# Kernel tuning notes

Measured on AMD Instinct MI355X. Metric: run time of the kernel, lower is better.

Reference implementation:

```python
import jax, jax.numpy as jnp
import numpy as np

N, E, G = 200000, 800000, 8192
IN, H, D, EXTRA = 128, 4, 64, 16


def setup_inputs() -> dict:
    key = jax.random.key(0)
    ks = jax.random.split(key, 24)
    inp = {
        'feats_node': jax.random.normal(ks[0], (N, IN), jnp.float32),
        'feats_graph': jax.random.normal(ks[1], (G, EXTRA), jnp.float32),
        'src': jax.random.randint(ks[2], (E,), 0, N, jnp.int32),
        'dst': jax.random.randint(ks[3], (E,), 0, N, jnp.int32),
        'graph_ids': jnp.sort(jax.random.randint(ks[4], (N,), 0, G, jnp.int32)),
        # GAT layer 1: fc [H*D, IN], attn [H, D], bias zeros (DGL default)
        'fc1_w': 0.5 * jax.random.normal(ks[5], (H * D, IN), jnp.float32),
        'attn_l1': 0.5 * jax.random.normal(ks[6], (H, D), jnp.float32),
        'attn_r1': 0.5 * jax.random.normal(ks[7], (H, D), jnp.float32),
        'bias1': jnp.zeros((H * D,), jnp.float32),
        # GAT layer 2
        'fc2_w': 0.5 * jax.random.normal(ks[8], (H * D, H * D), jnp.float32),
        'attn_l2': 0.5 * jax.random.normal(ks[9], (H, D), jnp.float32),
        'attn_r2': 0.5 * jax.random.normal(ks[10], (H, D), jnp.float32),
        'bias2': jnp.zeros((H * D,), jnp.float32),
        # GAT layer 3: 1 head
        'fc3_w': 0.5 * jax.random.normal(ks[11], (D, H * D), jnp.float32),
        'attn_l3': 0.5 * jax.random.normal(ks[12], (1, D), jnp.float32),
        'attn_r3': 0.5 * jax.random.normal(ks[13], (1, D), jnp.float32),
        'bias3': jnp.zeros((D,), jnp.float32),
        # readout score
        'score_w': 0.5 * jax.random.normal(ks[14], (1, D), jnp.float32),
        'score_b': jnp.zeros((1,), jnp.float32),
        # MLP: [D+EXTRA -> 2D -> D -> 1]
        'mlp_w1': 0.5 * jax.random.normal(ks[15], (2 * D, D + EXTRA), jnp.float32),
        'mlp_b1': jnp.zeros((2 * D,), jnp.float32),
        'mlp_w2': 0.5 * jax.random.normal(ks[16], (D, 2 * D), jnp.float32),
        'mlp_b2': jnp.zeros((D,), jnp.float32),
        'mlp_w3': 0.5 * jax.random.normal(ks[17], (1, D), jnp.float32),
        'mlp_b3': jnp.zeros((1,), jnp.float32),
    }
    return inp


def gat_conv(x, src, dst, fc_w, attn_l, attn_r, bias, n_heads, out_dim):
    # DGL GATConv: proj -> edge leaky_relu attention -> per-dst softmax -> aggregate
    n = x.shape[0]
    feat = (x @ fc_w.T).reshape(n, n_heads, out_dim)          # [N,H,D]
    el = jnp.einsum('nhd,hd->nh', feat, attn_l)               # [N,H]
    er = jnp.einsum('nhd,hd->nh', feat, attn_r)
    e = jax.nn.leaky_relu(el[src] + er[dst], 0.2)             # [E,H]
    m = jax.ops.segment_max(e, dst, num_segments=n)           # per-dst max
    m = jax.lax.stop_gradient(jnp.where(jnp.isfinite(m), m, 0.0))
    a = jnp.exp(e - m[dst])                                   # [E,H]
    denom = jax.ops.segment_sum(a, dst, num_segments=n)       # [N,H]
    alpha = a / jnp.where(denom[dst] == 0, 1.0, denom[dst])
    out = jax.ops.segment_sum(alpha[:, :, None] * feat[src], dst, num_segments=n)
    return out + bias.reshape(1, n_heads, out_dim)            # [N,H,D]


def reference(feats_node, feats_graph, src, dst, graph_ids,
              fc1_w, attn_l1, attn_r1, bias1,
              fc2_w, attn_l2, attn_r2, bias2,
              fc3_w, attn_l3, attn_r3, bias3,
              score_w, score_b,
              mlp_w1, mlp_b1, mlp_w2, mlp_b2, mlp_w3, mlp_b3):
    n = feats_node.shape[0]
    g = feats_graph.shape[0]
    x = jax.nn.selu(gat_conv(feats_node, src, dst, fc1_w, attn_l1, attn_r1, bias1, H, D)).reshape(n, H * D)
    x = jax.nn.selu(gat_conv(x, src, dst, fc2_w, attn_l2, attn_r2, bias2, H, D)).reshape(n, H * D)
    x = jax.nn.selu(gat_conv(x, src, dst, fc3_w, attn_l3, attn_r3, bias3, 1, D)).reshape(n, D)
    # weighted-average readout: sum(w*x)/sum(w) per graph
    w = jax.nn.sigmoid(x @ score_w.T + score_b)               # [N,1]
    num = jax.ops.segment_sum(w * x, graph_ids, num_segments=g)
    den = jax.ops.segment_sum(w, graph_ids, num_segments=g)
    emb = num / jnp.where(den == 0, 1.0, den)                 # [G,D]
    z = jnp.concatenate([emb, feats_graph], axis=1)           # [G,D+EXTRA]
    h = jax.nn.selu(z @ mlp_w1.T + mlp_b1)
    h = jax.nn.selu(h @ mlp_w2.T + mlp_b2)
    return h @ mlp_w3.T + mlp_b3                              # [G,1]
```

## Files before the change

kernel.cpp:

```cpp
#include <hip/hip_runtime.h>
#include <math.h>

#define N_NODES 200000
#define N_EDGES 800000
#define N_GRAPHS 8192
#define B1 16
#define B2 8
#define EC 128

typedef unsigned short ushort_t;

__device__ __forceinline__ float selu_f(float x){
  const float alpha = 1.6732632423543772f;
  const float lam   = 1.0507009873554805f;
  return x > 0.f ? lam * x : lam * alpha * (expf(x) - 1.f);
}

__global__ void zero_i32(int* p, int n){
  int i = blockIdx.x * 256 + threadIdx.x;
  if (i < n) p[i] = 0;
}

__global__ void deg_kernel(const int* __restrict__ dst, int* __restrict__ deg, int E){
  int e = blockIdx.x * 256 + threadIdx.x;
  if (e < E) atomicAdd(&deg[dst[e]], 1);
}

__global__ void scan1(const int* __restrict__ deg, int* __restrict__ rp, int* __restrict__ bs, int n){
  __shared__ int sh[256];
  int t = threadIdx.x;
  int base = blockIdx.x * 1024;
  int v[4]; int s = 0;
  #pragma unroll
  for (int i = 0; i < 4; i++){
    int idx = base + t * 4 + i;
    v[i] = (idx < n) ? deg[idx] : 0;
    s += v[i];
  }
  sh[t] = s; __syncthreads();
  for (int off = 1; off < 256; off <<= 1){
    int x = (t >= off) ? sh[t - off] : 0;
    __syncthreads();
    sh[t] += x;
    __syncthreads();
  }
  int run = (t == 0) ? 0 : sh[t - 1];
  #pragma unroll
  for (int i = 0; i < 4; i++){
    int idx = base + t * 4 + i;
    if (idx < n) rp[idx] = run;
    run += v[i];
  }
  if (t == 255) bs[blockIdx.x] = sh[255];
}

__global__ void scan2(int* bs, int nb){
  __shared__ int sh[256];
  int t = threadIdx.x;
  sh[t] = (t < nb) ? bs[t] : 0; __syncthreads();
  for (int off = 1; off < 256; off <<= 1){
    int x = (t >= off) ? sh[t - off] : 0;
    __syncthreads();
    sh[t] += x;
    __syncthreads();
  }
  int excl = (t == 0) ? 0 : sh[t - 1];
  if (t < nb) bs[t] = excl;
}

__global__ void scan3(int* rp, const int* __restrict__ bs, int n, int total){
  int i = blockIdx.x * 256 + threadIdx.x;
  if (i < n) rp[i] += bs[i >> 10];
  if (i == 0) rp[n] = total;
}

__global__ void fill_csr(const int* __restrict__ src, const int* __restrict__ dst,
                         const int* __restrict__ rp, int* __restrict__ fil,
                         int* __restrict__ csr, int E){
  int e = blockIdx.x * 256 + threadIdx.x;
  if (e < E){
    int d = dst[e];
    int p = atomicAdd(&fil[d], 1);
    csr[rp[d] + p] = src[e];
  }
}

__global__ void wt_kernel(const float* __restrict__ W1, const float* __restrict__ W2,
                          const float* __restrict__ W3,
                          float* __restrict__ W1t, float* __restrict__ W2t,
                          float* __restrict__ W3t){
  int i = blockIdx.x * 256 + threadIdx.x;
  if (i < 32768){
    int k = i >> 8, m = i & 255;
    W1t[i] = W1[(size_t)m * 128 + k];
  } else if (i < 32768 + 65536){
    int j = i - 32768;
    int k = j >> 8, m = j & 255;
    W2t[j] = W2[(size_t)m * 256 + k];
  } else if (i < 32768 + 65536 + 16384){
    int j = i - 32768 - 65536;
    int k = j >> 6, c = j & 63;
    W3t[j] = W3[(size_t)c * 256 + k];
  }
}

__global__ void compute_v(const float* __restrict__ W1, const float* __restrict__ al1, const float* __restrict__ ar1,
                          const float* __restrict__ W2, const float* __restrict__ al2, const float* __restrict__ ar2,
                          const float* __restrict__ W3, const float* __restrict__ al3, const float* __restrict__ ar3,
                          float* __restrict__ V1L, float* __restrict__ V1R,
                          float* __restrict__ V2L, float* __restrict__ V2R,
                          float* __restrict__ V3L, float* __restrict__ V3R){
  int i = blockIdx.x * 256 + threadIdx.x;
  if (i < 512){
    int h = i >> 7, k = i & 127;
    float sl = 0.f, sr = 0.f;
    for (int dd = 0; dd < 64; dd++){
      float w = W1[(size_t)(h * 64 + dd) * 128 + k];
      sl += al1[h * 64 + dd] * w;
      sr += ar1[h * 64 + dd] * w;
    }
    V1L[i] = sl; V1R[i] = sr;
  } else if (i < 1536){
    int j = i - 512;
    int h = j >> 8, k = j & 255;
    float sl = 0.f, sr = 0.f;
    for (int dd = 0; dd < 64; dd++){
      float w = W2[(size_t)(h * 64 + dd) * 256 + k];
      sl += al2[h * 64 + dd] * w;
      sr += ar2[h * 64 + dd] * w;
    }
    V2L[j] = sl; V2R[j] = sr;
  } else if (i < 1792){
    int k = i - 1536;
    float sl = 0.f, sr = 0.f;
    for (int dd = 0; dd < 64; dd++){
      float w = W3[(size_t)dd * 256 + k];
      sl += al3[dd] * w;
      sr += ar3[dd] * w;
    }
    V3L[k] = sl; V3R[k] = sr;
  }
}

__global__ __launch_bounds__(256) void el_er1(const float* __restrict__ x0,
                                              const float* __restrict__ V1L, const float* __restrict__ V1R,
                                              float* __restrict__ el1, float* __restrict__ er1, int n){
  __shared__ float vl[512], vr[512];
  int t = threadIdx.x;
  for (int i = t; i < 512; i += 256){ vl[i] = V1L[i]; vr[i] = V1R[i]; }
  __syncthreads();
  int node = blockIdx.x * 4 + (t >> 6);
  int l = t & 63;
  if (node >= n) return;
  float xa = x0[(size_t)node * 128 + l];
  float xb = x0[(size_t)node * 128 + 64 + l];
  #pragma unroll
  for (int h = 0; h < 4; h++){
    float pl = xa * vl[h * 128 + l] + xb * vl[h * 128 + 64 + l];
    float pr = xa * vr[h * 128 + l] + xb * vr[h * 128 + 64 + l];
    #pragma unroll
    for (int off = 32; off; off >>= 1){ pl += __shfl_xor(pl, off); pr += __shfl_xor(pr, off); }
    if (l == 0){ el1[(size_t)node * 4 + h] = pl; er1[(size_t)node * 4 + h] = pr; }
  }
}

__global__ __launch_bounds__(256) void alpha_h4(const float* __restrict__ el, const float* __restrict__ er,
                                                const int* __restrict__ rp, const int* __restrict__ csr,
                                                float* __restrict__ a, int n){
  int node = blockIdx.x * 256 + threadIdx.x;
  if (node >= n) return;
  int s0 = rp[node], s1 = rp[node + 1];
  if (s0 >= s1) return;
  float4 erv = *reinterpret_cast<const float4*>(er + (size_t)node * 4);
  float m0 = -1e30f, m1 = -1e30f, m2 = -1e30f, m3 = -1e30f;
  for (int i = s0; i < s1; i++){
    float4 e = *reinterpret_cast<const float4*>(el + (size_t)csr[i] * 4);
    float e0 = e.x + erv.x; e0 = e0 > 0.f ? e0 : 0.2f * e0; m0 = fmaxf(m0, e0);
    float e1 = e.y + erv.y; e1 = e1 > 0.f ? e1 : 0.2f * e1; m1 = fmaxf(m1, e1);
    float e2 = e.z + erv.z; e2 = e2 > 0.f ? e2 : 0.2f * e2; m2 = fmaxf(m2, e2);
    float e3 = e.w + erv.w; e3 = e3 > 0.f ? e3 : 0.2f * e3; m3 = fmaxf(m3, e3);
  }
  float d0 = 0.f, d1 = 0.f, d2 = 0.f, d3 = 0.f;
  for (int i = s0; i < s1; i++){
    float4 e = *reinterpret_cast<const float4*>(el + (size_t)csr[i] * 4);
    float e0 = e.x + erv.x; e0 = e0 > 0.f ? e0 : 0.2f * e0; d0 += expf(e0 - m0);
    float e1 = e.y + erv.y; e1 = e1 > 0.f ? e1 : 0.2f * e1; d1 += expf(e1 - m1);
    float e2 = e.z + erv.z; e2 = e2 > 0.f ? e2 : 0.2f * e2; d2 += expf(e2 - m2);
    float e3 = e.w + erv.w; e3 = e3 > 0.f ? e3 : 0.2f * e3; d3 += expf(e3 - m3);
  }
  d0 = 1.f / d0; d1 = 1.f / d1; d2 = 1.f / d2; d3 = 1.f / d3;
  for (int i = s0; i < s1; i++){
    float4 e = *reinterpret_cast<const float4*>(el + (size_t)csr[i] * 4);
    float4 o;
    float e0 = e.x + erv.x; e0 = e0 > 0.f ? e0 : 0.2f * e0; o.x = expf(e0 - m0) * d0;
    float e1 = e.y + erv.y; e1 = e1 > 0.f ? e1 : 0.2f * e1; o.y = expf(e1 - m1) * d1;
    float e2 = e.z + erv.z; e2 = e2 > 0.f ? e2 : 0.2f * e2; o.z = expf(e2 - m2) * d2;
    float e3 = e.w + erv.w; e3 = e3 > 0.f ? e3 : 0.2f * e3; o.w = expf(e3 - m3) * d3;
    *reinterpret_cast<float4*>(a + (size_t)i * 4) = o;
  }
}

__global__ __launch_bounds__(256) void alpha_h1(const float* __restrict__ el, const float* __restrict__ er,
                                                const int* __restrict__ rp, const int* __restrict__ csr,
                                                float* __restrict__ a, int n){
  int node = blockIdx.x * 256 + threadIdx.x;
  if (node >= n) return;
  int s0 = rp[node], s1 = rp[node + 1];
  if (s0 >= s1) return;
  float erv = er[node];
  float m = -1e30f;
  for (int i = s0; i < s1; i++){
    float e = el[csr[i]] + erv; e = e > 0.f ? e : 0.2f * e; m = fmaxf(m, e);
  }
  float den = 0.f;
  for (int i = s0; i < s1; i++){
    float e = el[csr[i]] + erv; e = e > 0.f ? e : 0.2f * e; den += expf(e - m);
  }
  float inv = 1.f / den;
  for (int i = s0; i < s1; i++){
    float e = el[csr[i]] + erv; e = e > 0.f ? e : 0.2f * e; a[i] = expf(e - m) * inv;
  }
}

__global__ __launch_bounds__(512, 2) void l1_fused(
    const float* __restrict__ x0, const float* __restrict__ W1t, const float* __restrict__ bias1,
    const float* __restrict__ a1,
    const float* __restrict__ V2L, const float* __restrict__ V2R,
    const int* __restrict__ rp, const int* __restrict__ csr,
    ushort_t* __restrict__ x1hi, unsigned char* __restrict__ x1lo,
    float* __restrict__ el2, float* __restrict__ er2){
  __shared__ float  aggT[4][129][20];
  __shared__ float  x1s[16][260];
  __shared__ float4 als4[EC];
  __shared__ int    ssrc[EC];
  __shared__ int    rpc[B1 + 1];
  int t = threadIdx.x;
  int nb0 = blockIdx.x * B1;
  if (t <= B1) rpc[t] = rp[nb0 + t];
  __syncthreads();
  int e0 = rpc[0], eN = rpc[B1];

  {
    int c = t & 127, g = t >> 7;
    float accr[4][4] = {{0.f}};
    for (int c0 = e0; c0 < eN; c0 += EC){
      int ce = min(EC, eN - c0);
      for (int i = t; i < ce; i += 512){
        ssrc[i] = csr[c0 + i];
        als4[i] = *reinterpret_cast<const float4*>(a1 + (size_t)(c0 + i) * 4);
      }
      __syncthreads();
      #pragma unroll
      for (int dd = 0; dd < 4; dd++){
        int d = g + dd * 4;
        int lo = max(rpc[d], c0) - c0;
        int hi = min(rpc[d + 1], c0 + ce) - c0;
        for (int i = lo; i < hi; i++){
          float xv = x0[(size_t)ssrc[i] * 128 + c];
          float4 av = als4[i];
          accr[dd][0] += av.x * xv;
          accr[dd][1] += av.y * xv;
          accr[dd][2] += av.z * xv;
          accr[dd][3] += av.w * xv;
        }
      }
      __syncthreads();
    }
    #pragma unroll
    for (int dd = 0; dd < 4; dd++){
      int d = g + dd * 4;
      aggT[0][c][d] = accr[dd][0];
      aggT[1][c][d] = accr[dd][1];
      aggT[2][c][d] = accr[dd][2];
      aggT[3][c][d] = accr[dd][3];
    }
  }
  __syncthreads();

  if (t < 256){
    int mt = t & 63, dt = t >> 6;
    int m0 = mt * 4, d0 = dt * 4, h = mt >> 4;
    float acc[4][4] = {{0.f}};
    #pragma unroll 4
    for (int k = 0; k < 128; k++){
      float4 w = *reinterpret_cast<const float4*>(W1t + (size_t)k * 256 + m0);
      float4 a = *reinterpret_cast<const float4*>(&aggT[h][k][d0]);
      acc[0][0] += a.x * w.x; acc[0][1] += a.x * w.y; acc[0][2] += a.x * w.z; acc[0][3] += a.x * w.w;
      acc[1][0] += a.y * w.x; acc[1][1] += a.y * w.y; acc[1][2] += a.y * w.z; acc[1][3] += a.y * w.w;
      acc[2][0] += a.z * w.x; acc[2][1] += a.z * w.y; acc[2][2] += a.z * w.z; acc[2][3] += a.z * w.w;
      acc[3][0] += a.w * w.x; acc[3][1] += a.w * w.y; acc[3][2] += a.w * w.z; acc[3][3] += a.w * w.w;
    }
    float4 b = *reinterpret_cast<const float4*>(bias1 + m0);
    #pragma unroll
    for (int i = 0; i < 4; i++){
      float4 v;
      v.x = selu_f(acc[i][0] + b.x);
      v.y = selu_f(acc[i][1] + b.y);
      v.z = selu_f(acc[i][2] + b.z);
      v.w = selu_f(acc[i][3] + b.w);
      *reinterpret_cast<float4*>(&x1s[d0 + i][m0]) = v;
      unsigned int ux = __float_as_uint(v.x), uy = __float_as_uint(v.y);
      unsigned int uz = __float_as_uint(v.z), uw = __float_as_uint(v.w);
      ushort4 h4; uchar4 l4;
      h4.x = (ushort_t)(ux >> 16); h4.y = (ushort_t)(uy >> 16);
      h4.z = (ushort_t)(uz >> 16); h4.w = (ushort_t)(uw >> 16);
      l4.x = (unsigned char)(ux >> 8); l4.y = (unsigned char)(uy >> 8);
      l4.z = (unsigned char)(uz >> 8); l4.w = (unsigned char)(uw >> 8);
      size_t base = (size_t)(nb0 + d0 + i) * 256 + m0;
      *reinterpret_cast<ushort4*>(x1hi + base) = h4;
      *reinterpret_cast<uchar4*>(x1lo + base) = l4;
    }
  }
  __syncthreads();

  if (t < 128){
    int d = t & 15, hq = (t >> 4) & 3, lr = t >> 6;
    const float* V = lr ? V2R : V2L;
    float p = 0.f;
    for (int k = 0; k < 256; k++) p += V[hq * 256 + k] * x1s[d][k];
    if (lr) er2[(size_t)(nb0 + d) * 4 + hq] = p;
    else    el2[(size_t)(nb0 + d) * 4 + hq] = p;
  }
}

__global__ __launch_bounds__(512, 2) void l2_fused(
    const ushort_t* __restrict__ x1hi, const unsigned char* __restrict__ x1lo,
    const float* __restrict__ W2t, const float* __restrict__ bias2,
    const float* __restrict__ a2, const float* __restrict__ W3t,
    const float* __restrict__ V3L, const float* __restrict__ V3R,
    const int* __restrict__ rp, const int* __restrict__ csr,
    float* __restrict__ feat3, float* __restrict__ el3, float* __restrict__ er3){
  __shared__ float  aggT[4][257][12];
  __shared__ float  x2s[8][260];
  __shared__ float4 als4[EC];
  __shared__ int    ssrc[EC];
  __shared__ int    rpc[B2 + 1];
  int t = threadIdx.x;
  int nb0 = blockIdx.x * B2;
  if (t <= B2) rpc[t] = rp[nb0 + t];
  __syncthreads();
  int e0 = rpc[0], eN = rpc[B2];

  {
    int c = t & 255, g = t >> 8;
    float accr[4][4] = {{0.f}};
    for (int c0 = e0; c0 < eN; c0 += EC){
      int ce = min(EC, eN - c0);
      for (int i = t; i < ce; i += 512){
        ssrc[i] = csr[c0 + i];
        als4[i] = *reinterpret_cast<const float4*>(a2 + (size_t)(c0 + i) * 4);
      }
      __syncthreads();
      #pragma unroll
      for (int dd = 0; dd < 4; dd++){
        int d = g * 4 + dd;
        int lo = max(rpc[d], c0) - c0;
        int hi = min(rpc[d + 1], c0 + ce) - c0;
        for (int i = lo; i < hi; i++){
          size_t s = (size_t)ssrc[i] * 256 + c;
          unsigned int u = ((unsigned int)x1hi[s] << 16) | ((unsigned int)x1lo[s] << 8);
          float xv = __uint_as_float(u);
          float4 av = als4[i];
          accr[dd][0] += av.x * xv;
          accr[dd][1] += av.y * xv;
          accr[dd][2] += av.z * xv;
          accr[dd][3] += av.w * xv;
        }
      }
      __syncthreads();
    }
    #pragma unroll
    for (int dd = 0; dd < 4; dd++){
      int d = g * 4 + dd;
      aggT[0][c][d] = accr[dd][0];
      aggT[1][c][d] = accr[dd][1];
      aggT[2][c][d] = accr[dd][2];
      aggT[3][c][d] = accr[dd][3];
    }
  }
  __syncthreads();

  if (t < 128){
    int mt = t & 63, dt = t >> 6;
    int m0 = mt * 4, d0 = dt * 4, h = mt >> 4;
    float acc[4][4] = {{0.f}};
    #pragma unroll 4
    for (int k = 0; k < 256; k++){
      float4 w = *reinterpret_cast<const float4*>(W2t + (size_t)k * 256 + m0);
      float4 a = *reinterpret_cast<const float4*>(&aggT[h][k][d0]);
      acc[0][0] += a.x * w.x; acc[0][1] += a.x * w.y; acc[0][2] += a.x * w.z; acc[0][3] += a.x * w.w;
      acc[1][0] += a.y * w.x; acc[1][1] += a.y * w.y; acc[1][2] += a.y * w.z; acc[1][3] += a.y * w.w;
      acc[2][0] += a.z * w.x; acc[2][1] += a.z * w.y; acc[2][2] += a.z * w.z; acc[2][3] += a.z * w.w;
      acc[3][0] += a.w * w.x; acc[3][1] += a.w * w.y; acc[3][2] += a.w * w.z; acc[3][3] += a.w * w.w;
    }
    float4 b = *reinterpret_cast<const float4*>(bias2 + m0);
    #pragma unroll
    for (int i = 0; i < 4; i++){
      float4 v;
      v.x = selu_f(acc[i][0] + b.x);
      v.y = selu_f(acc[i][1] + b.y);
      v.z = selu_f(acc[i][2] + b.z);
      v.w = selu_f(acc[i][3] + b.w);
      *reinterpret_cast<float4*>(&x2s[d0 + i][m0]) = v;
    }
  }
  __syncthreads();

  if (t >= 128 && t < 144){
    int j = t - 128;
    int d = j & 7, lr = j >> 3;
    const float* V = lr ? V3R : V3L;
    float p = 0.f;
    for (int k = 0; k < 256; k++) p += V[k] * x2s[d][k];
    if (lr) er3[nb0 + d] = p;
    else    el3[nb0 + d] = p;
  }
  if (t < 128){
    int mt = t & 15, d = t >> 4;
    int c0 = mt * 4;
    float a0 = 0.f, a1 = 0.f, a2r = 0.f, a3 = 0.f;
    #pragma unroll 4
    for (int k = 0; k < 256; k++){
      float4 w = *reinterpret_cast<const float4*>(W3t + (size_t)k * 64 + c0);
      float xv = x2s[d][k];
      a0 += xv * w.x; a1 += xv * w.y; a2r += xv * w.z; a3 += xv * w.w;
    }
    float4 o; o.x = a0; o.y = a1; o.z = a2r; o.w = a3;
    *reinterpret_cast<float4*>(feat3 + (size_t)(nb0 + d) * 64 + c0) = o;
  }
}

__global__ __launch_bounds__(256) void gat_agg3(const float* __restrict__ feat, const float* __restrict__ a3,
                                                const int* __restrict__ rp, const int* __restrict__ csr,
                                                const float* __restrict__ bias,
                                                float* __restrict__ out, int n){
  int node = blockIdx.x * 4 + (threadIdx.x >> 6);
  int t = threadIdx.x & 63;
  if (node >= n) return;
  int s0 = rp[node], s1 = rp[node + 1];
  float acc = 0.f;
  for (int i = s0; i < s1; i++){
    acc += a3[i] * feat[(size_t)csr[i] * 64 + t];
  }
  out[(size_t)node * 64 + t] = selu_f(acc + bias[t]);
}

__global__ void readout_kernel(const float* __restrict__ x3, const float* __restrict__ score_w,
                               const float* __restrict__ score_b, const int* __restrict__ gids,
                               float* __restrict__ num, float* __restrict__ den, int n){
  int node = blockIdx.x * 4 + (threadIdx.x >> 6);
  int lane = threadIdx.x & 63;
  if (node >= n) return;
  float xv = x3[(size_t)node * 64 + lane];
  float p = xv * score_w[lane];
  #pragma unroll
  for (int off = 32; off; off >>= 1) p += __shfl_xor(p, off);
  float w = 1.f / (1.f + expf(-(p + score_b[0])));
  int g = gids[node];
  atomicAdd(&num[(size_t)g * 64 + lane], w * xv);
  if (lane == 0) atomicAdd(&den[g], w);
}

__global__ __launch_bounds__(128) void mlp_kernel(
    const float* __restrict__ num, const float* __restrict__ den,
    const float* __restrict__ fg,
    const float* __restrict__ w1, const float* __restrict__ b1,
    const float* __restrict__ w2, const float* __restrict__ b2,
    const float* __restrict__ w3, const float* __restrict__ b3,
    float* __restrict__ out, int G){
  __shared__ float z[80];
  __shared__ float h1[128];
  __shared__ float h2[64];
  int t = threadIdx.x;
  for (int g = blockIdx.x; g < G; g += gridDim.x){
    if (t < 64){
      float d = den[g];
      d = (d == 0.f) ? 1.f : d;
      z[t] = num[(size_t)g * 64 + t] / d;
    } else if (t < 80){
      z[t] = fg[(size_t)g * 16 + (t - 64)];
    }
    __syncthreads();
    {
      float a = b1[t];
      for (int k = 0; k < 80; k++) a += z[k] * w1[t * 80 + k];
      h1[t] = selu_f(a);
    }
    __syncthreads();
    if (t < 64){
      float a = b2[t];
      for (int k = 0; k < 128; k++) a += h1[k] * w2[t * 128 + k];
      h2[t] = selu_f(a);
    }
    __syncthreads();
    if (t < 64){
      float p = h2[t] * w3[t];
      #pragma unroll
      for (int off = 32; off; off >>= 1) p += __shfl_down(p, off);
      if (t == 0) out[g] = p + b3[0];
    }
    __syncthreads();
  }
}

extern "C" void kernel_launch(void* const* d_in, const int* in_sizes, int n_in,
                              void* d_out, int out_size, void* d_ws, size_t ws_size,
                              hipStream_t stream) {
  const float* feats_node  = (const float*)d_in[0];
  const float* feats_graph = (const float*)d_in[1];
  const int*   src         = (const int*)d_in[2];
  const int*   dst         = (const int*)d_in[3];
  const int*   gids        = (const int*)d_in[4];
  const float* fc1_w   = (const float*)d_in[5];
  const float* attn_l1 = (const float*)d_in[6];
  const float* attn_r1 = (const float*)d_in[7];
  const float* bias1   = (const float*)d_in[8];
  const float* fc2_w   = (const float*)d_in[9];
  const float* attn_l2 = (const float*)d_in[10];
  const float* attn_r2 = (const float*)d_in[11];
  const float* bias2   = (const float*)d_in[12];
  const float* fc3_w   = (const float*)d_in[13];
  const float* attn_l3 = (const float*)d_in[14];
  const float* attn_r3 = (const float*)d_in[15];
  const float* bias3   = (const float*)d_in[16];
  const float* score_w = (const float*)d_in[17];
  const float* score_b = (const float*)d_in[18];
  const float* mlp_w1  = (const float*)d_in[19];
  const float* mlp_b1  = (const float*)d_in[20];
  const float* mlp_w2  = (const float*)d_in[21];
  const float* mlp_b2  = (const float*)d_in[22];
  const float* mlp_w3  = (const float*)d_in[23];
  const float* mlp_b3  = (const float*)d_in[24];
  float* out = (float*)d_out;

  char* ws = (char*)d_ws;
  size_t off = 0;
  auto alloc = [&](size_t bytes) -> void* {
    void* p = ws + off;
    off += (bytes + 255) / 256 * 256;
    return p;
  };
  int*   deg   = (int*)alloc((size_t)N_NODES * 4);
  int*   fil   = (int*)alloc((size_t)N_NODES * 4);
  int*   rp    = (int*)alloc((size_t)(N_NODES + 1) * 4);
  int*   bs    = (int*)alloc(256 * 4);
  int*   csr   = (int*)alloc((size_t)N_EDGES * 4);
  float* elbuf = (float*)alloc((size_t)N_NODES * 4 * 4);
  float* erbuf = (float*)alloc((size_t)N_NODES * 4 * 4);
  float* V1L   = (float*)alloc(512 * 4);
  float* V1R   = (float*)alloc(512 * 4);
  float* V2L   = (float*)alloc(1024 * 4);
  float* V2R   = (float*)alloc(1024 * 4);
  float* V3L   = (float*)alloc(256 * 4);
  float* V3R   = (float*)alloc(256 * 4);
  float* W1t   = (float*)alloc(32768 * 4);
  float* W2t   = (float*)alloc(65536 * 4);
  float* W3t   = (float*)alloc(16384 * 4);
  float* num   = (float*)alloc((size_t)N_GRAPHS * 64 * 4);
  float* den   = (float*)alloc((size_t)N_GRAPHS * 4);
  float* A     = (float*)alloc((size_t)N_EDGES * 4 * 4);
  float* feat3 = (float*)alloc((size_t)N_NODES * 64 * 4);
  ushort_t*      x1hi = (ushort_t*)alloc((size_t)N_NODES * 256 * 2);
  unsigned char* x1lo = (unsigned char*)alloc((size_t)N_NODES * 256);
  float* x3 = (float*)x1hi;

  zero_i32<<<(N_NODES + 255) / 256, 256, 0, stream>>>(deg, N_NODES);
  zero_i32<<<(N_NODES + 255) / 256, 256, 0, stream>>>(fil, N_NODES);
  zero_i32<<<(N_GRAPHS * 64 + 255) / 256, 256, 0, stream>>>((int*)num, N_GRAPHS * 64);
  zero_i32<<<(N_GRAPHS + 255) / 256, 256, 0, stream>>>((int*)den, N_GRAPHS);

  deg_kernel<<<(N_EDGES + 255) / 256, 256, 0, stream>>>(dst, deg, N_EDGES);
  scan1<<<196, 256, 0, stream>>>(deg, rp, bs, N_NODES);
  scan2<<<1, 256, 0, stream>>>(bs, 196);
  scan3<<<(N_NODES + 255) / 256, 256, 0, stream>>>(rp, bs, N_NODES, N_EDGES);
  fill_csr<<<(N_EDGES + 255) / 256, 256, 0, stream>>>(src, dst, rp, fil, csr, N_EDGES);

  compute_v<<<7, 256, 0, stream>>>(fc1_w, attn_l1, attn_r1, fc2_w, attn_l2, attn_r2,
                                   fc3_w, attn_l3, attn_r3, V1L, V1R, V2L, V2R, V3L, V3R);
  wt_kernel<<<448, 256, 0, stream>>>(fc1_w, fc2_w, fc3_w, W1t, W2t, W3t);
  el_er1<<<N_NODES / 4, 256, 0, stream>>>(feats_node, V1L, V1R, elbuf, erbuf, N_NODES);

  alpha_h4<<<(N_NODES + 255) / 256, 256, 0, stream>>>(elbuf, erbuf, rp, csr, A, N_NODES);
  l1_fused<<<N_NODES / B1, 512, 0, stream>>>(feats_node, W1t, bias1, A,
                                             V2L, V2R, rp, csr, x1hi, x1lo, elbuf, erbuf);
  alpha_h4<<<(N_NODES + 255) / 256, 256, 0, stream>>>(elbuf, erbuf, rp, csr, A, N_NODES);
  l2_fused<<<N_NODES / B2, 512, 0, stream>>>(x1hi, x1lo, W2t, bias2, A, W3t,
                                             V3L, V3R, rp, csr, feat3, elbuf, erbuf);
  alpha_h1<<<(N_NODES + 255) / 256, 256, 0, stream>>>(elbuf, erbuf, rp, csr, A, N_NODES);
  gat_agg3<<<N_NODES / 4, 256, 0, stream>>>(feat3, A, rp, csr, bias3, x3, N_NODES);

  readout_kernel<<<N_NODES / 4, 256, 0, stream>>>(x3, score_w, score_b, gids, num, den, N_NODES);
  mlp_kernel<<<256, 128, 0, stream>>>(num, den, feats_graph,
                                      mlp_w1, mlp_b1, mlp_w2, mlp_b2, mlp_w3, mlp_b3,
                                      out, N_GRAPHS);
}
```

Baseline: 2.766 ms.

## Restructure fused GAT layer kernels to per-node warp gathers and full-block GEMMs

Edge aggregation in the layer-1 and layer-2 fused kernels changes from chunked shared-memory staging of edge indices and attention weights to direct per-destination-node gathers. Each thread group handles one node and loads float4 (or packed hi/lo) feature vectors, with the next source index prefetched. The follow-on projection GEMMs are reorganised so all 512 threads participate, and layer 2 stages W2/W3 tiles through shared memory. This is meant to remove idle threads and block-wide barriers during the gather and the GEMM. In exchange, per-thread loop lengths now depend on node degree, and each aggT element is written by a single thread with possibly uncoalesced stores.

```diff
diff --git a/kernel.cpp b/kernel.cpp
--- a/kernel.cpp
+++ b/kernel.cpp
@@ -6,7 +6,6 @@
 #define N_GRAPHS 8192
 #define B1 16
 #define B2 8
-#define EC 128
 
 typedef unsigned short ushort_t;
 
@@ -229,76 +228,59 @@
     const int* __restrict__ rp, const int* __restrict__ csr,
     ushort_t* __restrict__ x1hi, unsigned char* __restrict__ x1lo,
     float* __restrict__ el2, float* __restrict__ er2){
-  __shared__ float  aggT[4][129][20];
-  __shared__ float  x1s[16][260];
-  __shared__ float4 als4[EC];
-  __shared__ int    ssrc[EC];
-  __shared__ int    rpc[B1 + 1];
+  __shared__ float aggT[4][128][20];
+  __shared__ float x1s[16][260];
   int t = threadIdx.x;
   int nb0 = blockIdx.x * B1;
-  if (t <= B1) rpc[t] = rp[nb0 + t];
+
+  {
+    int g = t >> 5;
+    int c4 = t & 31;
+    int i0 = rp[nb0 + g], i1 = rp[nb0 + g + 1];
+    float accr[4][4] = {{0.f}};
+    int s = (i0 < i1) ? csr[i0] : 0;
+    for (int i = i0; i < i1; i++){
+      int snext = (i + 1 < i1) ? csr[i + 1] : 0;
+      float4 av = *reinterpret_cast<const float4*>(a1 + (size_t)i * 4);
+      float4 xv = *reinterpret_cast<const float4*>(x0 + (size_t)s * 128 + c4 * 4);
+      accr[0][0] += av.x * xv.x; accr[0][1] += av.x * xv.y; accr[0][2] += av.x * xv.z; accr[0][3] += av.x * xv.w;
+      accr[1][0] += av.y * xv.x; accr[1][1] += av.y * xv.y; accr[1][2] += av.y * xv.z; accr[1][3] += av.y * xv.w;
+      accr[2][0] += av.z * xv.x; accr[2][1] += av.z * xv.y; accr[2][2] += av.z * xv.z; accr[2][3] += av.z * xv.w;
+      accr[3][0] += av.w * xv.x; accr[3][1] += av.w * xv.y; accr[3][2] += av.w * xv.z; accr[3][3] += av.w * xv.w;
+      s = snext;
+    }
+    #pragma unroll
+    for (int h = 0; h < 4; h++)
+      #pragma unroll
+      for (int j = 0; j < 4; j++)
+        aggT[h][c4 * 4 + j][g] = accr[h][j];
+  }
   __syncthreads();
-  int e0 = rpc[0], eN = rpc[B1];
 
   {
-    int c = t & 127, g = t >> 7;
-    float accr[4][4] = {{0.f}};
-    for (int c0 = e0; c0 < eN; c0 += EC){
-      int ce = min(EC, eN - c0);
-      for (int i = t; i < ce; i += 512){
-        ssrc[i] = csr[c0 + i];
-        als4[i] = *reinterpret_cast<const float4*>(a1 + (size_t)(c0 + i) * 4);
-      }
-      __syncthreads();
-      #pragma unroll
-      for (int dd = 0; dd < 4; dd++){
-        int d = g + dd * 4;
-        int lo = max(rpc[d], c0) - c0;
-        int hi = min(rpc[d + 1], c0 + ce) - c0;
-        for (int i = lo; i < hi; i++){
-          float xv = x0[(size_t)ssrc[i] * 128 + c];
-          float4 av = als4[i];
-          accr[dd][0] += av.x * xv;
-          accr[dd][1] += av.y * xv;
-          accr[dd][2] += av.z * xv;
-          accr[dd][3] += av.w * xv;
-        }
-      }
-      __syncthreads();
-    }
-    #pragma unroll
-    for (int dd = 0; dd < 4; dd++){
-      int d = g + dd * 4;
-      aggT[0][c][d] = accr[dd][0];
-      aggT[1][c][d] = accr[dd][1];
-      aggT[2][c][d] = accr[dd][2];
-      aggT[3][c][d] = accr[dd][3];
-    }
-  }
-  __syncthreads();
-
-  if (t < 256){
-    int mt = t & 63, dt = t >> 6;
-    int m0 = mt * 4, d0 = dt * 4, h = mt >> 4;
-    float acc[4][4] = {{0.f}};
+    int mt = t >> 3, dp = t & 7;
+    int m0 = mt * 4, h = mt >> 4;
+    float acc0[4] = {0.f, 0.f, 0.f, 0.f};
+    float acc1[4] = {0.f, 0.f, 0.f, 0.f};
     #pragma unroll 4
     for (int k = 0; k < 128; k++){
       float4 w = *reinterpret_cast<const float4*>(W1t + (size_t)k * 256 + m0);
-      float4 a = *reinterpret_cast<const float4*>(&aggT[h][k][d0]);
-      acc[0][0] += a.x * w.x; acc[0][1] += a.x * w.y; acc[0][2] += a.x * w.z; acc[0][3] += a.x * w.w;
-      acc[1][0] += a.y * w.x; acc[1][1] += a.y * w.y; acc[1][2] += a.y * w.z; acc[1][3] += a.y * w.w;
-      acc[2][0] += a.z * w.x; acc[2][1] += a.z * w.y; acc[2][2] += a.z * w.z; acc[2][3] += a.z * w.w;
-      acc[3][0] += a.w * w.x; acc[3][1] += a.w * w.y; acc[3][2] += a.w * w.z; acc[3][3] += a.w * w.w;
+      float a0 = aggT[h][k][dp];
+      float a1v = aggT[h][k][dp + 8];
+      acc0[0] += a0 * w.x; acc0[1] += a0 * w.y; acc0[2] += a0 * w.z; acc0[3] += a0 * w.w;
+      acc1[0] += a1v * w.x; acc1[1] += a1v * w.y; acc1[2] += a1v * w.z; acc1[3] += a1v * w.w;
     }
     float4 b = *reinterpret_cast<const float4*>(bias1 + m0);
     #pragma unroll
-    for (int i = 0; i < 4; i++){
+    for (int r = 0; r < 2; r++){
+      int d = dp + r * 8;
+      float* ac = r ? acc1 : acc0;
       float4 v;
-      v.x = selu_f(acc[i][0] + b.x);
-      v.y = selu_f(acc[i][1] + b.y);
-      v.z = selu_f(acc[i][2] + b.z);
-      v.w = selu_f(acc[i][3] + b.w);
-      *reinterpret_cast<float4*>(&x1s[d0 + i][m0]) = v;
+      v.x = selu_f(ac[0] + b.x);
+      v.y = selu_f(ac[1] + b.y);
+      v.z = selu_f(ac[2] + b.z);
+      v.w = selu_f(ac[3] + b.w);
+      *reinterpret_cast<float4*>(&x1s[d][m0]) = v;
       unsigned int ux = __float_as_uint(v.x), uy = __float_as_uint(v.y);
       unsigned int uz = __float_as_uint(v.z), uw = __float_as_uint(v.w);
       ushort4 h4; uchar4 l4;
@@ -306,7 +288,7 @@
       h4.z = (ushort_t)(uz >> 16); h4.w = (ushort_t)(uw >> 16);
       l4.x = (unsigned char)(ux >> 8); l4.y = (unsigned char)(uy >> 8);
       l4.z = (unsigned char)(uz >> 8); l4.w = (unsigned char)(uw >> 8);
-      size_t base = (size_t)(nb0 + d0 + i) * 256 + m0;
+      size_t base = (size_t)(nb0 + d) * 256 + m0;
       *reinterpret_cast<ushort4*>(x1hi + base) = h4;
       *reinterpret_cast<uchar4*>(x1lo + base) = l4;
     }
@@ -316,8 +298,14 @@
   if (t < 128){
     int d = t & 15, hq = (t >> 4) & 3, lr = t >> 6;
     const float* V = lr ? V2R : V2L;
+    const float4* Vq = reinterpret_cast<const float4*>(V + hq * 256);
+    const float4* Xq = reinterpret_cast<const float4*>(&x1s[d][0]);
     float p = 0.f;
-    for (int k = 0; k < 256; k++) p += V[hq * 256 + k] * x1s[d][k];
+    #pragma unroll 4
+    for (int q = 0; q < 64; q++){
+      float4 v = Vq[q]; float4 x = Xq[q];
+      p += v.x * x.x; p += v.y * x.y; p += v.z * x.z; p += v.w * x.w;
+    }
     if (lr) er2[(size_t)(nb0 + d) * 4 + hq] = p;
     else    el2[(size_t)(nb0 + d) * 4 + hq] = p;
   }
@@ -330,103 +318,103 @@
     const float* __restrict__ V3L, const float* __restrict__ V3R,
     const int* __restrict__ rp, const int* __restrict__ csr,
     float* __restrict__ feat3, float* __restrict__ el3, float* __restrict__ er3){
-  __shared__ float  aggT[4][257][12];
-  __shared__ float  x2s[8][260];
-  __shared__ float4 als4[EC];
-  __shared__ int    ssrc[EC];
-  __shared__ int    rpc[B2 + 1];
+  __shared__ float aggT[4][256][12];
+  __shared__ float Wst[4160];
+  __shared__ float x2s[8][260];
   int t = threadIdx.x;
   int nb0 = blockIdx.x * B2;
-  if (t <= B2) rpc[t] = rp[nb0 + t];
+
+  {
+    int d = t >> 6;
+    int c4 = t & 63;
+    int i0 = rp[nb0 + d], i1 = rp[nb0 + d + 1];
+    float accr[4][4] = {{0.f}};
+    int s = (i0 < i1) ? csr[i0] : 0;
+    for (int i = i0; i < i1; i++){
+      int snext = (i + 1 < i1) ? csr[i + 1] : 0;
+      float4 av = *reinterpret_cast<const float4*>(a2 + (size_t)i * 4);
+      ushort4 hv = *reinterpret_cast<const ushort4*>(x1hi + (size_t)s * 256 + c4 * 4);
+      uchar4  lv = *reinterpret_cast<const uchar4*>(x1lo + (size_t)s * 256 + c4 * 4);
+      float x0v = __uint_as_float(((unsigned int)hv.x << 16) | ((unsigned int)lv.x << 8));
+      float x1v = __uint_as_float(((unsigned int)hv.y << 16) | ((unsigned int)lv.y << 8));
+      float x2v = __uint_as_float(((unsigned int)hv.z << 16) | ((unsigned int)lv.z << 8));
+      float x3v = __uint_as_float(((unsigned int)hv.w << 16) | ((unsigned int)lv.w << 8));
+      accr[0][0] += av.x * x0v; accr[0][1] += av.x * x1v; accr[0][2] += av.x * x2v; accr[0][3] += av.x * x3v;
+      accr[1][0] += av.y * x0v; accr[1][1] += av.y * x1v; accr[1][2] += av.y * x2v; accr[1][3] += av.y * x3v;
+      accr[2][0] += av.z * x0v; accr[2][1] += av.z * x1v; accr[2][2] += av.z * x2v; accr[2][3] += av.z * x3v;
+      accr[3][0] += av.w * x0v; accr[3][1] += av.w * x1v; accr[3][2] += av.w * x2v; accr[3][3] += av.w * x3v;
+      s = snext;
+    }
+    #pragma unroll
+    for (int h = 0; h < 4; h++)
+      #pragma unroll
+      for (int j = 0; j < 4; j++)
+        aggT[h][c4 * 4 + j][d] = accr[h][j];
+  }
   __syncthreads();
-  int e0 = rpc[0], eN = rpc[B2];
 
   {
-    int c = t & 255, g = t >> 8;
-    float accr[4][4] = {{0.f}};
-    for (int c0 = e0; c0 < eN; c0 += EC){
-      int ce = min(EC, eN - c0);
-      for (int i = t; i < ce; i += 512){
-        ssrc[i] = csr[c0 + i];
-        als4[i] = *reinterpret_cast<const float4*>(a2 + (size_t)(c0 + i) * 4);
+    int mt = t >> 3, d2 = t & 7;
+    int m0 = mt * 4, h = mt >> 4;
+    float acc[4] = {0.f, 0.f, 0.f, 0.f};
+    int skr = t >> 5, sm = (t * 8) & 255;
+    for (int kc = 0; kc < 16; kc++){
+      {
+        const float* wsrc = W2t + (size_t)(kc * 16 + skr) * 256 + sm;
+        float4 wa = *reinterpret_cast<const float4*>(wsrc);
+        float4 wb = *reinterpret_cast<const float4*>(wsrc + 4);
+        *reinterpret_cast<float4*>(&Wst[skr * 260 + sm]) = wa;
+        *reinterpret_cast<float4*>(&Wst[skr * 260 + sm + 4]) = wb;
       }
       __syncthreads();
-      #pragma unroll
-      for (int dd = 0; dd < 4; dd++){
-        int d = g * 4 + dd;
-        int lo = max(rpc[d], c0) - c0;
-        int hi = min(rpc[d + 1], c0 + ce) - c0;
-        for (int i = lo; i < hi; i++){
-          size_t s = (size_t)ssrc[i] * 256 + c;
-          unsigned int u = ((unsigned int)x1hi[s] << 16) | ((unsigned int)x1lo[s] << 8);
-          float xv = __uint_as_float(u);
-          float4 av = als4[i];
-          accr[dd][0] += av.x * xv;
-          accr[dd][1] += av.y * xv;
-          accr[dd][2] += av.z * xv;
-          accr[dd][3] += av.w * xv;
-        }
+      #pragma unroll 4
+      for (int kr = 0; kr < 16; kr++){
+        int k = kc * 16 + kr;
+        float4 w = *reinterpret_cast<const float4*>(&Wst[kr * 260 + m0]);
+        float a = aggT[h][k][d2];
+        acc[0] += a * w.x; acc[1] += a * w.y; acc[2] += a * w.z; acc[3] += a * w.w;
       }
       __syncthreads();
     }
-    #pragma unroll
-    for (int dd = 0; dd < 4; dd++){
-      int d = g * 4 + dd;
-      aggT[0][c][d] = accr[dd][0];
-      aggT[1][c][d] = accr[dd][1];
-      aggT[2][c][d] = accr[dd][2];
-      aggT[3][c][d] = accr[dd][3];
-    }
+    float4 b = *reinterpret_cast<const float4*>(bias2 + m0);
+    float4 v;
+    v.x = selu_f(acc[0] + b.x);
+    v.y = selu_f(acc[1] + b.y);
+    v.z = selu_f(acc[2] + b.z);
+    v.w = selu_f(acc[3] + b.w);
+    *reinterpret_cast<float4*>(&x2s[d2][m0]) = v;
   }
   __syncthreads();
 
-  if (t < 128){
-    int mt = t & 63, dt = t >> 6;
-    int m0 = mt * 4, d0 = dt * 4, h = mt >> 4;
-    float acc[4][4] = {{0.f}};
-    #pragma unroll 4
-    for (int k = 0; k < 256; k++){
-      float4 w = *reinterpret_cast<const float4*>(W2t + (size_t)k * 256 + m0);
-      float4 a = *reinterpret_cast<const float4*>(&aggT[h][k][d0]);
-      acc[0][0] += a.x * w.x; acc[0][1] += a.x * w.y; acc[0][2] += a.x * w.z; acc[0][3] += a.x * w.w;
-      acc[1][0] += a.y * w.x; acc[1][1] += a.y * w.y; acc[1][2] += a.y * w.z; acc[1][3] += a.y * w.w;
-      acc[2][0] += a.z * w.x; acc[2][1] += a.z * w.y; acc[2][2] += a.z * w.z; acc[2][3] += a.z * w.w;
-      acc[3][0] += a.w * w.x; acc[3][1] += a.w * w.y; acc[3][2] += a.w * w.z; acc[3][3] += a.w * w.w;
-    }
-    float4 b = *reinterpret_cast<const float4*>(bias2 + m0);
-    #pragma unroll
-    for (int i = 0; i < 4; i++){
-      float4 v;
-      v.x = selu_f(acc[i][0] + b.x);
-      v.y = selu_f(acc[i][1] + b.y);
-      v.z = selu_f(acc[i][2] + b.z);
-      v.w = selu_f(acc[i][3] + b.w);
-      *reinterpret_cast<float4*>(&x2s[d0 + i][m0]) = v;
-    }
-  }
-  __syncthreads();
-
-  if (t >= 128 && t < 144){
-    int j = t - 128;
-    int d = j & 7, lr = j >> 3;
+  {
+    int d3 = t >> 6, c = t & 63;
+    float acc = 0.f;
+    int skr = t >> 3, sc = (t * 8) & 63;
+    for (int kc = 0; kc < 4; kc++){
+      __syncthreads();
+      {
+        const float* wsrc = W3t + (size_t)(kc * 64 + skr) * 64 + sc;
+        float4 wa = *reinterpret_cast<const float4*>(wsrc);
+        float4 wb = *reinterpret_cast<const float4*>(wsrc + 4);
+        *reinterpret_cast<float4*>(&Wst[skr * 64 + sc]) = wa;
+        *reinterpret_cast<float4*>(&Wst[skr * 64 + sc + 4]) = wb;
+      }
+      __syncthreads();
+      #pragma unroll 8
+      for (int kr = 0; kr < 64; kr++){
+        acc += Wst[kr * 64 + c] * x2s[d3][kc * 64 + kr];
+      }
+    }
+    feat3[(size_t)(nb0 + d3) * 64 + c] = acc;
+  }
+
+  if (t < 16){
+    int d = t & 7, lr = t >> 3;
     const float* V = lr ? V3R : V3L;
     float p = 0.f;
     for (int k = 0; k < 256; k++) p += V[k] * x2s[d][k];
     if (lr) er3[nb0 + d] = p;
     else    el3[nb0 + d] = p;
-  }
-  if (t < 128){
-    int mt = t & 15, d = t >> 4;
-    int c0 = mt * 4;
-    float a0 = 0.f, a1 = 0.f, a2r = 0.f, a3 = 0.f;
-    #pragma unroll 4
-    for (int k = 0; k < 256; k++){
-      float4 w = *reinterpret_cast<const float4*>(W3t + (size_t)k * 64 + c0);
-      float xv = x2s[d][k];
-      a0 += xv * w.x; a1 += xv * w.y; a2r += xv * w.z; a3 += xv * w.w;
-    }
-    float4 o; o.x = a0; o.y = a1; o.z = a2r; o.w = a3;
-    *reinterpret_cast<float4*>(feat3 + (size_t)(nb0 + d) * 64 + c0) = o;
   }
 }
 
@@ -439,8 +427,11 @@
   if (node >= n) return;
   int s0 = rp[node], s1 = rp[node + 1];
   float acc = 0.f;
-  for (int i = s0; i < s1; i++){
-    acc += a3[i] * feat[(size_t)csr[i] * 64 + t];
+  int s = (s0 < s1) ? csr[s0] : 0;
+  for (int i = s0; i < s1; i++){
+    int snext = (i + 1 < s1) ? csr[i + 1] : 0;
+    acc += a3[i] * feat[(size_t)s * 64 + t];
+    s = snext;
   }
   out[(size_t)node * 64 + t] = selu_f(acc + bias[t]);
 }
```

New measurement: 2.597 ms. -6.1%, faster.
